# Performance work log

Measured on AMD Instinct MI355X. Metric: run time of the kernel, lower is better.

The kernel has to match this reference:

```python
import jax, jax.numpy as jnp
import numpy as np

N, D, NUM_CLASSES = 8192, 256, 512
DELTA = 1.0


def setup_inputs() -> dict:
    key = jax.random.key(0)
    k1, k2 = jax.random.split(key)
    queries = jax.random.normal(k1, (N, D), dtype=jnp.float32)
    targets = jax.random.randint(k2, (N,), 0, NUM_CLASSES, dtype=jnp.int64)
    return {"queries": queries, "targets": targets}


def _mine(queries, targets):
    # Pairwise squared L2 distances via gram expansion (avoids [N,N,D] intermediate).
    sq = jnp.sum(queries * queries, axis=-1)              # [N]
    dist = sq[:, None] + sq[None, :] - 2.0 * (queries @ queries.T)  # [N,N]
    same = targets[:, None] == targets[None, :]           # [N,N] bool
    diag = jnp.eye(dist.shape[0], dtype=bool)
    neg_inf = jnp.float32(-jnp.inf)
    # hardest positive: argmax over (distances * same_mask) with -inf diagonal
    pos_masked = jnp.where(diag, neg_inf, dist * same)
    pos_idx = jnp.argmax(pos_masked, axis=-1)
    # original: (-(distances * ~same, diag=-inf)).argmin == argmax of the masked matrix
    neg_masked = jnp.where(diag, neg_inf, dist * (~same))
    neg_idx = jnp.argmax(neg_masked, axis=-1)
    return pos_idx, neg_idx


def reference(queries, targets):
    pos_idx, neg_idx = _mine(queries, targets)
    pos = queries[pos_idx]                                # [N,D]
    neg = queries[neg_idx]                                # [N,D]
    d_pos = jnp.sum((queries - pos) ** 2, axis=-1, keepdims=True)  # [N,1]
    d_neg = jnp.sum((queries - neg) ** 2, axis=-1, keepdims=True)  # [N,1]
    loss = jax.nn.relu(DELTA - d_pos + d_neg)
    return jnp.mean(loss)
```

## Files before the change

kernel.cpp:

```cpp
#include <hip/hip_runtime.h>

#define N 8192
#define D 256
#define NB 64
#define NTILES (NB * (NB + 1) / 2)

typedef _Float16 f16x8 __attribute__((ext_vector_type(8)));
typedef float f32x4 __attribute__((ext_vector_type(4)));

__device__ __forceinline__ void gload16(const void* g, void* lds) {
    __builtin_amdgcn_global_load_lds(
        (const __attribute__((address_space(1))) void*)g,
        (__attribute__((address_space(3))) void*)lds, 16, 0, 0);
}


__global__ __launch_bounds__(256) void prep_kernel(const float* __restrict__ q,
                                                   _Float16* __restrict__ qh,
                                                   float* __restrict__ sq,
                                                   unsigned* __restrict__ pos_key,
                                                   unsigned* __restrict__ neg_key,
                                                   float* __restrict__ out) {
    const int row = blockIdx.x * 4 + (threadIdx.x >> 6);
    const int lane = threadIdx.x & 63;
    if (threadIdx.x < 8) {
        const int r0 = blockIdx.x * 4 + (threadIdx.x >> 1);
        if (threadIdx.x & 1) neg_key[r0] = 0u; else pos_key[r0] = 0u;
    }
    if (blockIdx.x == 0 && threadIdx.x == 0) out[0] = 0.0f;
    const float4 v = ((const float4*)(q + row * D))[lane];
    _Float16 h[4];
    h[0] = (_Float16)v.x; h[1] = (_Float16)v.y;
    h[2] = (_Float16)v.z; h[3] = (_Float16)v.w;
    *(short4*)(qh + row * D + lane * 4) = *(const short4*)h;
    float s = v.x * v.x + v.y * v.y + v.z * v.z + v.w * v.w;
    #pragma unroll
    for (int off = 32; off; off >>= 1) s += __shfl_down(s, off, 64);
    if (lane == 0) sq[row] = s;
}

__global__ __launch_bounds__(256, 3) void mine_kernel(
    const _Float16* __restrict__ qh, const int* __restrict__ tgt,
    const float* __restrict__ sqv,
    unsigned* __restrict__ pos_key, unsigned* __restrict__ neg_key)
{
    __shared__ char smem[33792];
    __shared__ float sqI[128], sqJ[128];
    __shared__ int   tgI[128], tgJ[128];

    _Float16* A0 = (_Float16*)smem;
    _Float16* A1 = A0 + 128 * 32;
    _Float16* B0 = A1 + 128 * 32;
    _Float16* B1 = B0 + 128 * 32;
    unsigned* mpos = (unsigned*)smem;
    unsigned* mneg = (unsigned*)(smem + 16896);

    int tt = blockIdx.x, bi = 0;
    while (tt >= NB - bi) { tt -= NB - bi; ++bi; }
    const int bj = bi + tt;
    const int i0 = bi * 128, j0 = bj * 128;
    const bool diag = (bi == bj);

    const int tid = threadIdx.x;
    const int w = tid >> 6, lane = tid & 63;
    const int quad = lane >> 4, lc = lane & 15;
    const int wy = w >> 1, wx = w & 1;

    if (tid < 128) { sqI[tid] = sqv[i0 + tid]; tgI[tid] = tgt[i0 + tid]; }
    else { const int c = tid - 128; sqJ[c] = sqv[j0 + c]; tgJ[c] = tgt[j0 + c]; }
    __syncthreads();

    float sqjn[4];
    #pragma unroll
    for (int nt = 0; nt < 4; ++nt) sqjn[nt] = sqJ[wx * 64 + nt * 16 + lc];
    f32x4 acc[4][4];
    #pragma unroll
    for (int mt = 0; mt < 4; ++mt) {
        const f32x4 si4 = *(const f32x4*)&sqI[wy * 64 + mt * 16 + quad * 4];
        #pragma unroll
        for (int nt = 0; nt < 4; ++nt)
            #pragma unroll
            for (int r = 0; r < 4; ++r)
                acc[mt][nt][r] = -0.5f * (si4[r] + sqjn[nt]);
    }

    for (int c = 0; c < D / 64; ++c) {
        const int dk = c * 64;
        __syncthreads();
        #pragma unroll
        for (int it = 0; it < 2; ++it) {
            const int s = it * 256 + tid;
            const int r = s >> 2, sub = (s & 3) * 8;
            const int lbase = (it * 256 + w * 64) * 16;
            const size_t ga = (size_t)(i0 + r) * D + dk + sub;
            gload16(qh + ga,      (char*)A0 + lbase);
            gload16(qh + ga + 32, (char*)A1 + lbase);
            if (!diag) {
                const size_t gb = (size_t)(j0 + r) * D + dk + sub;
                gload16(qh + gb,      (char*)B0 + lbase);
                gload16(qh + gb + 32, (char*)B1 + lbase);
            }
        }
        __syncthreads();

        #pragma unroll
        for (int kk = 0; kk < 2; ++kk) {
            const _Float16* AP = kk ? A1 : A0;
            const _Float16* BP = diag ? AP : (kk ? B1 : B0);
            f16x8 fb[4];
            #pragma unroll
            for (int t = 0; t < 4; ++t)
                fb[t] = *(const f16x8*)&BP[(wx * 64 + t * 16 + lc) * 32 + quad * 8];
            #pragma unroll
            for (int mt = 0; mt < 4; ++mt) {
                const f16x8 fa = *(const f16x8*)&AP[(wy * 64 + mt * 16 + lc) * 32 + quad * 8];
                #pragma unroll
                for (int nt = 0; nt < 4; ++nt)
                    acc[mt][nt] = __builtin_amdgcn_mfma_f32_16x16x32_f16(
                        fa, fb[nt], acc[mt][nt], 0, 0, 0);
            }
        }
    }

    __syncthreads();

    int tj[4]; unsigned jc[4], jpk[4], jnk[4];
    #pragma unroll
    for (int nt = 0; nt < 4; ++nt) {
        const int cl = wx * 64 + nt * 16 + lc;
        tj[nt] = tgJ[cl];
        jc[nt] = 0x1FFFu - (unsigned)(j0 + cl);
        jpk[nt] = 0u; jnk[nt] = 0u;
    }

    #pragma unroll
    for (int mt = 0; mt < 4; ++mt) {
        const int rbase = wy * 64 + mt * 16 + quad * 4;
        const int4 ti4 = *(const int4*)&tgI[rbase];
        #pragma unroll
        for (int r = 0; r < 4; ++r) {
            const int sr = rbase + r;
            const unsigned rk = 0x1FFFu - (unsigned)(i0 + sr);
            const int ti = ((const int*)&ti4)[r];
            unsigned bpk = 0u, bnk = 0u;
            #pragma unroll
            for (int nt = 0; nt < 4; ++nt) {
                const int cl = wx * 64 + nt * 16 + lc;
                const float dist = fmaxf(-2.0f * acc[mt][nt][r], 0.0f);
                const unsigned db = __float_as_uint(dist) & 0xFFFFE000u;
                const bool same = (ti == tj[nt]);
                const bool dia = diag && (sr == cl);
                const unsigned pb = dia ? 0u : (same ? db : 0u);
                const unsigned nb = dia ? 0u : (same ? 0u : db);
                bpk = max(bpk, dia ? 0u : (pb | jc[nt]));
                bnk = max(bnk, dia ? 0u : (nb | jc[nt]));
                jpk[nt] = max(jpk[nt], dia ? 0u : (pb | rk));
                jnk[nt] = max(jnk[nt], dia ? 0u : (nb | rk));
            }
            mpos[sr * 33 + wx * 16 + lc] = bpk;
            mneg[sr * 33 + wx * 16 + lc] = bnk;
        }
    }
    __syncthreads();

    {
        const int sr = tid & 127;
        const unsigned* m = (tid < 128) ? &mpos[sr * 33] : &mneg[sr * 33];
        unsigned best = 0u;
        #pragma unroll
        for (int k = 0; k < 32; ++k) best = max(best, m[k]);
        unsigned* gk = (tid < 128) ? pos_key : neg_key;
        atomicMax(&gk[i0 + sr], best);
    }

    if (!diag) {
        #pragma unroll
        for (int nt = 0; nt < 4; ++nt) {
            unsigned pk = jpk[nt], nk = jnk[nt];
            #pragma unroll
            for (int off = 16; off < 64; off <<= 1) {
                pk = max(pk, (unsigned)__shfl_xor((int)pk, off, 64));
                nk = max(nk, (unsigned)__shfl_xor((int)nk, off, 64));
            }
            if (quad == 0) {
                const int gcol = j0 + wx * 64 + nt * 16 + lc;
                atomicMax(&pos_key[gcol], pk);
                atomicMax(&neg_key[gcol], nk);
            }
        }
    }
}

__global__ __launch_bounds__(256) void final_kernel(
    const float* __restrict__ q, const unsigned* __restrict__ pos_key,
    const unsigned* __restrict__ neg_key, float* __restrict__ out)
{
    __shared__ float red[4];
    const int wv = threadIdx.x >> 6, lane = threadIdx.x & 63;
    float wsum = 0.0f;
    for (int rr = 0; rr < 32; ++rr) {
        const int row = (blockIdx.x * 4 + wv) * 32 + rr;
        const int bpi = 0x1FFF - (int)(pos_key[row] & 0x1FFFu);
        const int bni = 0x1FFF - (int)(neg_key[row] & 0x1FFFu);
        const float4 qi = ((const float4*)(q + row * D))[lane];
        const float4 qp = ((const float4*)(q + (size_t)bpi * D))[lane];
        const float4 qn = ((const float4*)(q + (size_t)bni * D))[lane];
        float dx, dp = 0.0f, dn = 0.0f;
        dx = qi.x - qp.x; dp += dx * dx;
        dx = qi.y - qp.y; dp += dx * dx;
        dx = qi.z - qp.z; dp += dx * dx;
        dx = qi.w - qp.w; dp += dx * dx;
        dx = qi.x - qn.x; dn += dx * dx;
        dx = qi.y - qn.y; dn += dx * dx;
        dx = qi.z - qn.z; dn += dx * dx;
        dx = qi.w - qn.w; dn += dx * dx;
        #pragma unroll
        for (int off = 32; off; off >>= 1) {
            dp += __shfl_down(dp, off, 64);
            dn += __shfl_down(dn, off, 64);
        }
        if (lane == 0) wsum += fmaxf(0.0f, (1.0f - dp) + dn);
    }
    if (lane == 0) red[wv] = wsum;
    __syncthreads();
    if (threadIdx.x == 0)
        atomicAdd(out, (red[0] + red[1] + red[2] + red[3]) * (1.0f / N));
}

extern "C" void kernel_launch(void* const* d_in, const int* in_sizes, int n_in,
                              void* d_out, int out_size, void* d_ws, size_t ws_size,
                              hipStream_t stream) {
    const float* q = (const float*)d_in[0];
    const int* tgt = (const int*)d_in[1];
    float* out = (float*)d_out;

    unsigned* pos_key = (unsigned*)d_ws;
    unsigned* neg_key = pos_key + N;
    _Float16* qh = (_Float16*)(neg_key + N);
    float* sqv = (float*)(qh + (size_t)N * D);

    prep_kernel<<<dim3(N / 4), dim3(256), 0, stream>>>(q, qh, sqv, pos_key, neg_key, out);
    mine_kernel<<<dim3(NTILES), dim3(256), 0, stream>>>(qh, tgt, sqv, pos_key, neg_key);
    final_kernel<<<dim3(64), dim3(256), 0, stream>>>(q, pos_key, neg_key, out);
}
```

Baseline: 110.4 us.

## Load MFMA operands directly from global memory instead of staging through LDS

The LDS-staged loop is removed: it used global_load_lds double-buffered chunks and two barriers per chunk. Each wave now reads its f16x8 A and B fragments straight from global memory (through cache) for every 32-wide K step, and the per-chunk __syncthreads are gone. This cuts barrier overhead and shrinks the shared buffer, since mpos/mneg become standalone arrays. In exchange, each operand row is reread by multiple waves from L1/L2 rather than shared in LDS, and the load latency is exposed directly to the MFMA chain.

```diff
diff --git a/kernel.cpp b/kernel.cpp
--- a/kernel.cpp
+++ b/kernel.cpp
@@ -7,12 +7,6 @@
 
 typedef _Float16 f16x8 __attribute__((ext_vector_type(8)));
 typedef float f32x4 __attribute__((ext_vector_type(4)));
-
-__device__ __forceinline__ void gload16(const void* g, void* lds) {
-    __builtin_amdgcn_global_load_lds(
-        (const __attribute__((address_space(1))) void*)g,
-        (__attribute__((address_space(3))) void*)lds, 16, 0, 0);
-}
 
 
 __global__ __launch_bounds__(256) void prep_kernel(const float* __restrict__ q,
@@ -44,16 +38,9 @@
     const float* __restrict__ sqv,
     unsigned* __restrict__ pos_key, unsigned* __restrict__ neg_key)
 {
-    __shared__ char smem[33792];
+    __shared__ unsigned mpos[128 * 33], mneg[128 * 33];
     __shared__ float sqI[128], sqJ[128];
     __shared__ int   tgI[128], tgJ[128];
-
-    _Float16* A0 = (_Float16*)smem;
-    _Float16* A1 = A0 + 128 * 32;
-    _Float16* B0 = A1 + 128 * 32;
-    _Float16* B1 = B0 + 128 * 32;
-    unsigned* mpos = (unsigned*)smem;
-    unsigned* mneg = (unsigned*)(smem + 16896);
 
     int tt = blockIdx.x, bi = 0;
     while (tt >= NB - bi) { tt -= NB - bi; ++bi; }
@@ -70,6 +57,14 @@
     else { const int c = tid - 128; sqJ[c] = sqv[j0 + c]; tgJ[c] = tgt[j0 + c]; }
     __syncthreads();
 
+    const _Float16* pa[4];
+    const _Float16* pb[4];
+    #pragma unroll
+    for (int t = 0; t < 4; ++t) {
+        pa[t] = qh + (size_t)(i0 + wy * 64 + t * 16 + lc) * D + quad * 8;
+        pb[t] = qh + (size_t)(j0 + wx * 64 + t * 16 + lc) * D + quad * 8;
+    }
+
     float sqjn[4];
     #pragma unroll
     for (int nt = 0; nt < 4; ++nt) sqjn[nt] = sqJ[wx * 64 + nt * 16 + lc];
@@ -84,45 +79,21 @@
                 acc[mt][nt][r] = -0.5f * (si4[r] + sqjn[nt]);
     }
 
-    for (int c = 0; c < D / 64; ++c) {
-        const int dk = c * 64;
-        __syncthreads();
-        #pragma unroll
-        for (int it = 0; it < 2; ++it) {
-            const int s = it * 256 + tid;
-            const int r = s >> 2, sub = (s & 3) * 8;
-            const int lbase = (it * 256 + w * 64) * 16;
-            const size_t ga = (size_t)(i0 + r) * D + dk + sub;
-            gload16(qh + ga,      (char*)A0 + lbase);
-            gload16(qh + ga + 32, (char*)A1 + lbase);
-            if (!diag) {
-                const size_t gb = (size_t)(j0 + r) * D + dk + sub;
-                gload16(qh + gb,      (char*)B0 + lbase);
-                gload16(qh + gb + 32, (char*)B1 + lbase);
-            }
-        }
-        __syncthreads();
-
-        #pragma unroll
-        for (int kk = 0; kk < 2; ++kk) {
-            const _Float16* AP = kk ? A1 : A0;
-            const _Float16* BP = diag ? AP : (kk ? B1 : B0);
-            f16x8 fb[4];
-            #pragma unroll
-            for (int t = 0; t < 4; ++t)
-                fb[t] = *(const f16x8*)&BP[(wx * 64 + t * 16 + lc) * 32 + quad * 8];
-            #pragma unroll
-            for (int mt = 0; mt < 4; ++mt) {
-                const f16x8 fa = *(const f16x8*)&AP[(wy * 64 + mt * 16 + lc) * 32 + quad * 8];
-                #pragma unroll
-                for (int nt = 0; nt < 4; ++nt)
-                    acc[mt][nt] = __builtin_amdgcn_mfma_f32_16x16x32_f16(
-                        fa, fb[nt], acc[mt][nt], 0, 0, 0);
-            }
-        }
-    }
-
-    __syncthreads();
+    #pragma unroll 2
+    for (int c = 0; c < D / 32; ++c) {
+        const int ko = c * 32;
+        f16x8 fb[4];
+        #pragma unroll
+        for (int t = 0; t < 4; ++t) fb[t] = *(const f16x8*)(pb[t] + ko);
+        #pragma unroll
+        for (int mt = 0; mt < 4; ++mt) {
+            const f16x8 fa = *(const f16x8*)(pa[mt] + ko);
+            #pragma unroll
+            for (int nt = 0; nt < 4; ++nt)
+                acc[mt][nt] = __builtin_amdgcn_mfma_f32_16x16x32_f16(
+                    fa, fb[nt], acc[mt][nt], 0, 0, 0);
+        }
+    }
 
     int tj[4]; unsigned jc[4], jpk[4], jnk[4];
     #pragma unroll
@@ -150,12 +121,12 @@
                 const unsigned db = __float_as_uint(dist) & 0xFFFFE000u;
                 const bool same = (ti == tj[nt]);
                 const bool dia = diag && (sr == cl);
-                const unsigned pb = dia ? 0u : (same ? db : 0u);
-                const unsigned nb = dia ? 0u : (same ? 0u : db);
-                bpk = max(bpk, dia ? 0u : (pb | jc[nt]));
-                bnk = max(bnk, dia ? 0u : (nb | jc[nt]));
-                jpk[nt] = max(jpk[nt], dia ? 0u : (pb | rk));
-                jnk[nt] = max(jnk[nt], dia ? 0u : (nb | rk));
+                const unsigned pb_ = dia ? 0u : (same ? db : 0u);
+                const unsigned nb_ = dia ? 0u : (same ? 0u : db);
+                bpk = max(bpk, dia ? 0u : (pb_ | jc[nt]));
+                bnk = max(bnk, dia ? 0u : (nb_ | jc[nt]));
+                jpk[nt] = max(jpk[nt], dia ? 0u : (pb_ | rk));
+                jnk[nt] = max(jnk[nt], dia ? 0u : (nb_ | rk));
             }
             mpos[sr * 33 + wx * 16 + lc] = bpk;
             mneg[sr * 33 + wx * 16 + lc] = bnk;
```

Measured after the change: 153.1 us. 1.39x slower.
